# Optimization experiments

Measured on AMD Instinct MI355X. Metric: run time of the kernel, lower is better.

## Reference

```python
import jax, jax.numpy as jnp
import numpy as np

INPUT_DIM = 2048
NUM_EXPERTS = 64
TOP_K = 2


def setup_inputs() -> dict:
    key = jax.random.key(0)
    kx, kw = jax.random.split(key)
    x = jax.random.normal(kx, (4, 4096, INPUT_DIM), dtype=jnp.float32)
    # nn.Linear weight has shape [num_experts, input_dim]
    W = jax.random.normal(kw, (NUM_EXPERTS, INPUT_DIM), dtype=jnp.float32) * (INPUT_DIM ** -0.5)
    return {"x": x, "W": W}


def reference(x, W):
    # Flatten tokens: [N, D]
    x_flat = x.reshape(-1, INPUT_DIM)
    # Gate logits: [N, E]
    gate_logits = jnp.einsum("nd,ed->ne", x_flat, W)
    # Top-k (sorted descending, matching torch.topk)
    top_k_logits, top_k_indices = jax.lax.top_k(gate_logits, TOP_K)
    top_k_values = jax.nn.softmax(top_k_logits, axis=-1)
    return (top_k_indices, top_k_values)
```

## Files before the change

### kernel.cpp

```cpp
#include <hip/hip_runtime.h>
#include <hip/hip_bf16.h>
#include <math.h>

typedef float f4 __attribute__((ext_vector_type(4)));
typedef float f32x4 __attribute__((ext_vector_type(4)));
typedef short bf16x8 __attribute__((ext_vector_type(8)));
typedef unsigned int u32x4 __attribute__((ext_vector_type(4)));

#define D      2048
#define NE     64
#define TOKB   16
#define KSPLIT 8
#define KRNG   (D / KSPLIT)
#define KCH    32
#define NCH    (KRNG / KCH)
#define CSTR   68

__device__ __forceinline__ unsigned short bf16rne(float f) {
    unsigned int u = __builtin_bit_cast(unsigned int, f);
    u += 0x7fffu + ((u >> 16) & 1u);
    return (unsigned short)(u >> 16);
}
__device__ __forceinline__ float bf2f(unsigned short h) {
    unsigned int u = (unsigned int)h << 16;
    return __builtin_bit_cast(float, u);
}

__global__ __launch_bounds__(256)
void wprep(const float* __restrict__ W,
           unsigned short* __restrict__ Whp,
           unsigned short* __restrict__ Wlp)
{
    const int i  = blockIdx.x * 256 + threadIdx.x;
    const int j  = i & 7;
    const int l  = (i >> 3) & 63;
    const int et = (i >> 9) & 3;
    const int kc = i >> 11;
    const int e  = et * 16 + (l & 15);
    const int k  = kc * 32 + (l >> 4) * 8 + j;
    const float w = W[(size_t)e * D + k];
    const unsigned short h = bf16rne(w);
    Whp[i] = h;
    Wlp[i] = bf16rne(w - bf2f(h));
}

#define CVTPAIR(F0, F1, HOUT, LOUT) {                                        \
    __hip_bfloat162 hp_ = __float22bfloat162_rn(make_float2((F0), (F1)));    \
    unsigned hu_; __builtin_memcpy(&hu_, &hp_, 4);                           \
    const float h0_ = __builtin_bit_cast(float, hu_ << 16);                  \
    const float h1_ = __builtin_bit_cast(float, hu_ & 0xffff0000u);          \
    __hip_bfloat162 lp_ = __float22bfloat162_rn(                             \
        make_float2((F0) - h0_, (F1) - h1_));                                \
    unsigned lu_; __builtin_memcpy(&lu_, &lp_, 4);                           \
    HOUT = hu_;                                                              \
    LOUT = lu_;                                                              \
}

__global__ __launch_bounds__(512, 6)
void moe_fused(const float* __restrict__ x,
               const unsigned short* __restrict__ Whp,
               const unsigned short* __restrict__ Wlp,
               float* __restrict__ out, int ntok)
{
    __shared__ float cred[KSPLIT][TOKB * CSTR];

    const int t    = threadIdx.x;
    const int w    = t >> 6;
    const int l    = t & 63;
    const int tok0 = blockIdx.x * TOKB;

    const int ar  = l & 15;
    const int akb = (l >> 4) * 8;

    const float* xa = x + (size_t)(tok0 + ar) * D + w * KRNG + akb;
    const unsigned short* whp = Whp + (size_t)w * 16384 + l * 8;
    const unsigned short* wlp = Wlp + (size_t)w * 16384 + l * 8;

#define LOADX(ch, R0, R1) { \
    const float* p_ = xa + (ch) * KCH; \
    R0 = *(const f4*)(p_);     \
    R1 = *(const f4*)(p_ + 4); }

#define CHUNK(ch, R0, R1) { \
    bf16x8 bh[4], bl[4]; \
    _Pragma("unroll") \
    for (int et = 0; et < 4; ++et) { \
        const size_t o_ = (size_t)(4 * (ch) + et) * 512; \
        bh[et] = *(const bf16x8*)(whp + o_); \
        bl[et] = *(const bf16x8*)(wlp + o_); \
    } \
    unsigned hu0_, hu1_, hu2_, hu3_, lu0_, lu1_, lu2_, lu3_; \
    CVTPAIR(R0.x, R0.y, hu0_, lu0_); \
    CVTPAIR(R0.z, R0.w, hu1_, lu1_); \
    CVTPAIR(R1.x, R1.y, hu2_, lu2_); \
    CVTPAIR(R1.z, R1.w, hu3_, lu3_); \
    const u32x4 hv_ = {hu0_, hu1_, hu2_, hu3_}; \
    const u32x4 lv_ = {lu0_, lu1_, lu2_, lu3_}; \
    const bf16x8 ah = __builtin_bit_cast(bf16x8, hv_); \
    const bf16x8 al = __builtin_bit_cast(bf16x8, lv_); \
    if ((ch) + 2 < NCH) LOADX((ch) + 2, R0, R1); \
    _Pragma("unroll") \
    for (int et = 0; et < 4; ++et) { \
        acc[et] = __builtin_amdgcn_mfma_f32_16x16x32_bf16(ah, bh[et], acc[et], 0, 0, 0); \
        acc[et] = __builtin_amdgcn_mfma_f32_16x16x32_bf16(ah, bl[et], acc[et], 0, 0, 0); \
        acc[et] = __builtin_amdgcn_mfma_f32_16x16x32_bf16(al, bh[et], acc[et], 0, 0, 0); \
    } }

    const f32x4 zz = {0.f, 0.f, 0.f, 0.f};
    f32x4 acc[4] = {zz, zz, zz, zz};

    f4 xE0, xE1, xO0, xO1;

    LOADX(0, xE0, xE1);
    LOADX(1, xO0, xO1);

#pragma unroll
    for (int ch = 0; ch < NCH; ch += 2) {
        CHUNK(ch,     xE0, xE1);
        CHUNK(ch + 1, xO0, xO1);
    }

#undef LOADX
#undef CHUNK

#pragma unroll
    for (int et = 0; et < 4; ++et)
#pragma unroll
        for (int r = 0; r < 4; ++r) {
            const int tokl = (l >> 4) * 4 + r;
            cred[w][tokl * CSTR + et * 16 + (l & 15)] = acc[et][r];
        }
    __syncthreads();

    if (t < TOKB * 8) {
        const int tokl = t >> 3;
        const int eg   = t & 7;
        f4 s0 = {0.f,0.f,0.f,0.f}, s1 = {0.f,0.f,0.f,0.f};
#pragma unroll
        for (int ww = 0; ww < KSPLIT; ++ww) {
            const float* cw = &cred[ww][tokl * CSTR + eg * 8];
            s0 += *(const f4*)cw;
            s1 += *(const f4*)(cw + 4);
        }
        const float vv[8] = {s0.x, s0.y, s0.z, s0.w, s1.x, s1.y, s1.z, s1.w};
        float m1 = -INFINITY, m2 = -INFINITY;
        int i1 = 0, i2 = 0;
#pragma unroll
        for (int j = 0; j < 8; ++j) {
            const float v = vv[j];
            const int id = eg * 8 + j;
            if (v > m1)      { m2 = m1; i2 = i1; m1 = v; i1 = id; }
            else if (v > m2) { m2 = v;  i2 = id; }
        }
#pragma unroll
        for (int m = 1; m < 8; m <<= 1) {
            const float om1 = __shfl_xor(m1, m);
            const int   oi1 = __shfl_xor(i1, m);
            const float om2 = __shfl_xor(m2, m);
            const int   oi2 = __shfl_xor(i2, m);
            const bool b1 = (om1 > m1) || (om1 == m1 && oi1 < i1);
            const float c2v = b1 ? m1 : om1;  const int c2i = b1 ? i1 : oi1;
            const float c3v = b1 ? om2 : m2;  const int c3i = b1 ? oi2 : i2;
            if (b1) { m1 = om1; i1 = oi1; }
            const bool b2 = (c3v > c2v) || (c3v == c2v && c3i < c2i);
            m2 = b2 ? c3v : c2v;  i2 = b2 ? c3i : c2i;
        }
        if (eg == 0) {
            const int tok = tok0 + tokl;
            out[(size_t)tok * 2 + 0] = (float)i1;
            out[(size_t)tok * 2 + 1] = (float)i2;
            const float p1 = 1.0f / (1.0f + expf(m2 - m1));
            float* vals = out + (size_t)ntok * 2;
            vals[(size_t)tok * 2 + 0] = p1;
            vals[(size_t)tok * 2 + 1] = 1.0f - p1;
        }
    }
}

extern "C" void kernel_launch(void* const* d_in, const int* in_sizes, int n_in,
                              void* d_out, int out_size, void* d_ws, size_t ws_size,
                              hipStream_t stream)
{
    const float* x = (const float*)d_in[0];
    const float* W = (const float*)d_in[1];
    float* out = (float*)d_out;
    unsigned short* Whp = (unsigned short*)d_ws;
    unsigned short* Wlp = Whp + (size_t)NE * D;

    const int ntok = in_sizes[0] / D;
    wprep<<<(NE * D) / 256, 256, 0, stream>>>(W, Whp, Wlp);
    moe_fused<<<ntok / TOKB, 512, 0, stream>>>(x, Whp, Wlp, out, ntok);
}
```

Measured before the change: 46.24 us.

## Software-pipeline W and x loads with inline asm and explicit vmcnt waits

Replaces the compiler-scheduled loads in the main loop with inline-asm global_load_dwordx4 issues, double-buffering the weight fragments for the next chunk and keeping x loads two chunks ahead. Explicit s_waitcnt vmcnt(10) waits with sched barriers let the MFMAs of the current chunk overlap outstanding loads. The occupancy hint drops from 6 to 4 waves per SIMD to make room for the extra registers. Risks include wrong vmcnt accounting when the number of loads issued changes at the tail, and lower latency hiding from reduced occupancy.

```diff
diff --git a/kernel.cpp b/kernel.cpp
--- a/kernel.cpp
+++ b/kernel.cpp
@@ -56,7 +56,15 @@
     LOUT = lu_;                                                              \
 }
 
-__global__ __launch_bounds__(512, 6)
+#define GL16(dst, ptr) \
+    asm volatile("global_load_dwordx4 %0, %1, off" : "=v"(dst) : "v"(ptr) : "memory")
+
+#define WAIT10 { asm volatile("s_waitcnt vmcnt(10)" ::: "memory"); \
+                 __builtin_amdgcn_sched_barrier(0); }
+#define WAIT0  { asm volatile("s_waitcnt vmcnt(0)"  ::: "memory"); \
+                 __builtin_amdgcn_sched_barrier(0); }
+
+__global__ __launch_bounds__(512, 4)
 void moe_fused(const float* __restrict__ x,
                const unsigned short* __restrict__ Whp,
                const unsigned short* __restrict__ Wlp,
@@ -76,19 +84,28 @@
     const unsigned short* whp = Whp + (size_t)w * 16384 + l * 8;
     const unsigned short* wlp = Wlp + (size_t)w * 16384 + l * 8;
 
-#define LOADX(ch, R0, R1) { \
-    const float* p_ = xa + (ch) * KCH; \
-    R0 = *(const f4*)(p_);     \
-    R1 = *(const f4*)(p_ + 4); }
-
-#define CHUNK(ch, R0, R1) { \
-    bf16x8 bh[4], bl[4]; \
-    _Pragma("unroll") \
-    for (int et = 0; et < 4; ++et) { \
-        const size_t o_ = (size_t)(4 * (ch) + et) * 512; \
-        bh[et] = *(const bf16x8*)(whp + o_); \
-        bl[et] = *(const bf16x8*)(wlp + o_); \
-    } \
+    const f32x4 zz = {0.f, 0.f, 0.f, 0.f};
+    f32x4 acc[4] = {zz, zz, zz, zz};
+
+    bf16x8 bEh0, bEh1, bEh2, bEh3, bEl0, bEl1, bEl2, bEl3;
+    bf16x8 bOh0, bOh1, bOh2, bOh3, bOl0, bOl1, bOl2, bOl3;
+    f4 xE0, xE1, xO0, xO1;
+
+#define BISSUE(CH, S) { \
+    GL16(b##S##h0, whp + (size_t)(4*(CH)+0)*512); \
+    GL16(b##S##l0, wlp + (size_t)(4*(CH)+0)*512); \
+    GL16(b##S##h1, whp + (size_t)(4*(CH)+1)*512); \
+    GL16(b##S##l1, wlp + (size_t)(4*(CH)+1)*512); \
+    GL16(b##S##h2, whp + (size_t)(4*(CH)+2)*512); \
+    GL16(b##S##l2, wlp + (size_t)(4*(CH)+2)*512); \
+    GL16(b##S##h3, whp + (size_t)(4*(CH)+3)*512); \
+    GL16(b##S##l3, wlp + (size_t)(4*(CH)+3)*512); }
+
+#define XISSUE(CH, R0, R1) { \
+    GL16(R0, xa + (CH) * KCH);     \
+    GL16(R1, xa + (CH) * KCH + 4); }
+
+#define CVTA(R0, R1) \
     unsigned hu0_, hu1_, hu2_, hu3_, lu0_, lu1_, lu2_, lu3_; \
     CVTPAIR(R0.x, R0.y, hu0_, lu0_); \
     CVTPAIR(R0.z, R0.w, hu1_, lu1_); \
@@ -97,31 +114,60 @@
     const u32x4 hv_ = {hu0_, hu1_, hu2_, hu3_}; \
     const u32x4 lv_ = {lu0_, lu1_, lu2_, lu3_}; \
     const bf16x8 ah = __builtin_bit_cast(bf16x8, hv_); \
-    const bf16x8 al = __builtin_bit_cast(bf16x8, lv_); \
-    if ((ch) + 2 < NCH) LOADX((ch) + 2, R0, R1); \
-    _Pragma("unroll") \
-    for (int et = 0; et < 4; ++et) { \
-        acc[et] = __builtin_amdgcn_mfma_f32_16x16x32_bf16(ah, bh[et], acc[et], 0, 0, 0); \
-        acc[et] = __builtin_amdgcn_mfma_f32_16x16x32_bf16(ah, bl[et], acc[et], 0, 0, 0); \
-        acc[et] = __builtin_amdgcn_mfma_f32_16x16x32_bf16(al, bh[et], acc[et], 0, 0, 0); \
-    } }
-
-    const f32x4 zz = {0.f, 0.f, 0.f, 0.f};
-    f32x4 acc[4] = {zz, zz, zz, zz};
-
-    f4 xE0, xE1, xO0, xO1;
-
-    LOADX(0, xE0, xE1);
-    LOADX(1, xO0, xO1);
-
-#pragma unroll
-    for (int ch = 0; ch < NCH; ch += 2) {
-        CHUNK(ch,     xE0, xE1);
-        CHUNK(ch + 1, xO0, xO1);
-    }
-
-#undef LOADX
-#undef CHUNK
+    const bf16x8 al = __builtin_bit_cast(bf16x8, lv_);
+
+#define MFMAS(S) { \
+    acc[0] = __builtin_amdgcn_mfma_f32_16x16x32_bf16(ah, b##S##h0, acc[0], 0, 0, 0); \
+    acc[0] = __builtin_amdgcn_mfma_f32_16x16x32_bf16(ah, b##S##l0, acc[0], 0, 0, 0); \
+    acc[0] = __builtin_amdgcn_mfma_f32_16x16x32_bf16(al, b##S##h0, acc[0], 0, 0, 0); \
+    acc[1] = __builtin_amdgcn_mfma_f32_16x16x32_bf16(ah, b##S##h1, acc[1], 0, 0, 0); \
+    acc[1] = __builtin_amdgcn_mfma_f32_16x16x32_bf16(ah, b##S##l1, acc[1], 0, 0, 0); \
+    acc[1] = __builtin_amdgcn_mfma_f32_16x16x32_bf16(al, b##S##h1, acc[1], 0, 0, 0); \
+    acc[2] = __builtin_amdgcn_mfma_f32_16x16x32_bf16(ah, b##S##h2, acc[2], 0, 0, 0); \
+    acc[2] = __builtin_amdgcn_mfma_f32_16x16x32_bf16(ah, b##S##l2, acc[2], 0, 0, 0); \
+    acc[2] = __builtin_amdgcn_mfma_f32_16x16x32_bf16(al, b##S##h2, acc[2], 0, 0, 0); \
+    acc[3] = __builtin_amdgcn_mfma_f32_16x16x32_bf16(ah, b##S##h3, acc[3], 0, 0, 0); \
+    acc[3] = __builtin_amdgcn_mfma_f32_16x16x32_bf16(ah, b##S##l3, acc[3], 0, 0, 0); \
+    acc[3] = __builtin_amdgcn_mfma_f32_16x16x32_bf16(al, b##S##h3, acc[3], 0, 0, 0); }
+
+#define ITER_FULL(CH, S, OS, R0, R1) { \
+    BISSUE((CH) + 1, OS) \
+    WAIT10 \
+    CVTA(R0, R1) \
+    XISSUE((CH) + 2, R0, R1) \
+    MFMAS(S) }
+
+#define ITER_NOX(CH, S, OS, R0, R1) { \
+    BISSUE((CH) + 1, OS) \
+    WAIT10 \
+    CVTA(R0, R1) \
+    MFMAS(S) }
+
+#define ITER_LAST(CH, S, R0, R1) { \
+    WAIT0 \
+    CVTA(R0, R1) \
+    MFMAS(S) }
+
+    BISSUE(0, E)
+    XISSUE(0, xE0, xE1)
+    XISSUE(1, xO0, xO1)
+
+    ITER_FULL(0, E, O, xE0, xE1)
+    ITER_FULL(1, O, E, xO0, xO1)
+    ITER_FULL(2, E, O, xE0, xE1)
+    ITER_FULL(3, O, E, xO0, xO1)
+    ITER_FULL(4, E, O, xE0, xE1)
+    ITER_FULL(5, O, E, xO0, xO1)
+    ITER_NOX (6, E, O, xE0, xE1)
+    ITER_LAST(7, O, xO0, xO1)
+
+#undef BISSUE
+#undef XISSUE
+#undef CVTA
+#undef MFMAS
+#undef ITER_FULL
+#undef ITER_NOX
+#undef ITER_LAST
 
 #pragma unroll
     for (int et = 0; et < 4; ++et)
```

Result: no change. 45.52 us (-1.5%).

## Split gating GEMM into split-K kernel with LDS-shared weights plus top-2 pass

Applied to the files above, without the earlier changes.

The fused kernel is split into two kernels. The first is a split-K GEMM in which each 512-thread block covers 128 tokens (16 per wave) over one K slice. The block's W hi/lo slice is staged once in LDS with global_load_lds and shared by all eight waves, instead of every wave reading its own weights from global memory. Partial logits for each K slice go to a global workspace, and a second kernel sums the slices and performs top-2 plus softmax. This cuts redundant weight traffic per token, but adds a partial-sum round trip of 8x the logit size through global memory and one more kernel launch.

```diff
diff --git a/kernel.cpp b/kernel.cpp
--- a/kernel.cpp
+++ b/kernel.cpp
@@ -9,12 +9,16 @@
 
 #define D      2048
 #define NE     64
-#define TOKB   16
-#define KSPLIT 8
-#define KRNG   (D / KSPLIT)
+#define TPW    16
+#define NWAVE  8
+#define TOKB   (TPW * NWAVE)
+#define KS     8
+#define KRNG   (D / KS)
 #define KCH    32
 #define NCH    (KRNG / KCH)
-#define CSTR   68
+
+#define AS1C(p) ((const __attribute__((address_space(1))) void*)(p))
+#define AS3(p)  ((__attribute__((address_space(3))) void*)(p))
 
 __device__ __forceinline__ unsigned short bf16rne(float f) {
     unsigned int u = __builtin_bit_cast(unsigned int, f);
@@ -56,39 +60,51 @@
     LOUT = lu_;                                                              \
 }
 
-__global__ __launch_bounds__(512, 6)
-void moe_fused(const float* __restrict__ x,
-               const unsigned short* __restrict__ Whp,
-               const unsigned short* __restrict__ Wlp,
-               float* __restrict__ out, int ntok)
-{
-    __shared__ float cred[KSPLIT][TOKB * CSTR];
+__global__ __launch_bounds__(512, 4)
+void moe_gemm(const float* __restrict__ x,
+              const unsigned short* __restrict__ Whp,
+              const unsigned short* __restrict__ Wlp,
+              float* __restrict__ part, int ntok)
+{
+    __shared__ unsigned short Wlds[NCH][4][2][512];
 
     const int t    = threadIdx.x;
     const int w    = t >> 6;
     const int l    = t & 63;
-    const int tok0 = blockIdx.x * TOKB;
+    const int mbc  = ntok / TOKB;
+    const int mb   = blockIdx.x % mbc;
+    const int ks   = blockIdx.x / mbc;
+    const int tok0 = mb * TOKB;
 
     const int ar  = l & 15;
     const int akb = (l >> 4) * 8;
 
-    const float* xa = x + (size_t)(tok0 + ar) * D + w * KRNG + akb;
-    const unsigned short* whp = Whp + (size_t)w * 16384 + l * 8;
-    const unsigned short* wlp = Wlp + (size_t)w * 16384 + l * 8;
-
-#define LOADX(ch, R0, R1) { \
-    const float* p_ = xa + (ch) * KCH; \
-    R0 = *(const f4*)(p_);     \
-    R1 = *(const f4*)(p_ + 4); }
-
-#define CHUNK(ch, R0, R1) { \
-    bf16x8 bh[4], bl[4]; \
-    _Pragma("unroll") \
-    for (int et = 0; et < 4; ++et) { \
-        const size_t o_ = (size_t)(4 * (ch) + et) * 512; \
-        bh[et] = *(const bf16x8*)(whp + o_); \
-        bl[et] = *(const bf16x8*)(wlp + o_); \
-    } \
+    {
+        const size_t kcg = (size_t)(ks * NCH + w) * 4;
+#pragma unroll
+        for (int et = 0; et < 4; ++et) {
+            __builtin_amdgcn_global_load_lds(
+                AS1C(Whp + (kcg + et) * 512 + l * 8),
+                AS3(&Wlds[w][et][0][0]), 16, 0, 0);
+            __builtin_amdgcn_global_load_lds(
+                AS1C(Wlp + (kcg + et) * 512 + l * 8),
+                AS3(&Wlds[w][et][1][0]), 16, 0, 0);
+        }
+    }
+
+    const float* xa = x + (size_t)(tok0 + w * TPW + ar) * D + ks * KRNG + akb;
+
+    f4 xE0 = *(const f4*)(xa);
+    f4 xE1 = *(const f4*)(xa + 4);
+    f4 xO0 = *(const f4*)(xa + KCH);
+    f4 xO1 = *(const f4*)(xa + KCH + 4);
+
+    __syncthreads();
+
+    const f32x4 zz = {0.f, 0.f, 0.f, 0.f};
+    f32x4 acc[4] = {zz, zz, zz, zz};
+
+#define CVTA(R0, R1) \
     unsigned hu0_, hu1_, hu2_, hu3_, lu0_, lu1_, lu2_, lu3_; \
     CVTPAIR(R0.x, R0.y, hu0_, lu0_); \
     CVTPAIR(R0.z, R0.w, hu1_, lu1_); \
@@ -97,83 +113,86 @@
     const u32x4 hv_ = {hu0_, hu1_, hu2_, hu3_}; \
     const u32x4 lv_ = {lu0_, lu1_, lu2_, lu3_}; \
     const bf16x8 ah = __builtin_bit_cast(bf16x8, hv_); \
-    const bf16x8 al = __builtin_bit_cast(bf16x8, lv_); \
-    if ((ch) + 2 < NCH) LOADX((ch) + 2, R0, R1); \
+    const bf16x8 al = __builtin_bit_cast(bf16x8, lv_);
+
+#define CHUNK(CH, R0, R1, REFILL) { \
+    CVTA(R0, R1) \
+    if (REFILL) { R0 = *(const f4*)(xa + ((CH) + 2) * KCH); \
+                  R1 = *(const f4*)(xa + ((CH) + 2) * KCH + 4); } \
     _Pragma("unroll") \
     for (int et = 0; et < 4; ++et) { \
-        acc[et] = __builtin_amdgcn_mfma_f32_16x16x32_bf16(ah, bh[et], acc[et], 0, 0, 0); \
-        acc[et] = __builtin_amdgcn_mfma_f32_16x16x32_bf16(ah, bl[et], acc[et], 0, 0, 0); \
-        acc[et] = __builtin_amdgcn_mfma_f32_16x16x32_bf16(al, bh[et], acc[et], 0, 0, 0); \
+        const bf16x8 bh = *(const bf16x8*)&Wlds[CH][et][0][l * 8]; \
+        const bf16x8 bl = *(const bf16x8*)&Wlds[CH][et][1][l * 8]; \
+        acc[et] = __builtin_amdgcn_mfma_f32_16x16x32_bf16(ah, bh, acc[et], 0, 0, 0); \
+        acc[et] = __builtin_amdgcn_mfma_f32_16x16x32_bf16(ah, bl, acc[et], 0, 0, 0); \
+        acc[et] = __builtin_amdgcn_mfma_f32_16x16x32_bf16(al, bh, acc[et], 0, 0, 0); \
     } }
 
-    const f32x4 zz = {0.f, 0.f, 0.f, 0.f};
-    f32x4 acc[4] = {zz, zz, zz, zz};
-
-    f4 xE0, xE1, xO0, xO1;
-
-    LOADX(0, xE0, xE1);
-    LOADX(1, xO0, xO1);
-
-#pragma unroll
-    for (int ch = 0; ch < NCH; ch += 2) {
-        CHUNK(ch,     xE0, xE1);
-        CHUNK(ch + 1, xO0, xO1);
-    }
-
-#undef LOADX
+    CHUNK(0, xE0, xE1, 1)
+    CHUNK(1, xO0, xO1, 1)
+    CHUNK(2, xE0, xE1, 1)
+    CHUNK(3, xO0, xO1, 1)
+    CHUNK(4, xE0, xE1, 1)
+    CHUNK(5, xO0, xO1, 1)
+    CHUNK(6, xE0, xE1, 0)
+    CHUNK(7, xO0, xO1, 0)
+
+#undef CVTA
 #undef CHUNK
 
+    float* pp = part + ((size_t)ks * ntok + tok0 + w * TPW) * NE;
 #pragma unroll
     for (int et = 0; et < 4; ++et)
 #pragma unroll
-        for (int r = 0; r < 4; ++r) {
-            const int tokl = (l >> 4) * 4 + r;
-            cred[w][tokl * CSTR + et * 16 + (l & 15)] = acc[et][r];
-        }
-    __syncthreads();
-
-    if (t < TOKB * 8) {
-        const int tokl = t >> 3;
-        const int eg   = t & 7;
-        f4 s0 = {0.f,0.f,0.f,0.f}, s1 = {0.f,0.f,0.f,0.f};
-#pragma unroll
-        for (int ww = 0; ww < KSPLIT; ++ww) {
-            const float* cw = &cred[ww][tokl * CSTR + eg * 8];
-            s0 += *(const f4*)cw;
-            s1 += *(const f4*)(cw + 4);
-        }
-        const float vv[8] = {s0.x, s0.y, s0.z, s0.w, s1.x, s1.y, s1.z, s1.w};
-        float m1 = -INFINITY, m2 = -INFINITY;
-        int i1 = 0, i2 = 0;
-#pragma unroll
-        for (int j = 0; j < 8; ++j) {
-            const float v = vv[j];
-            const int id = eg * 8 + j;
-            if (v > m1)      { m2 = m1; i2 = i1; m1 = v; i1 = id; }
-            else if (v > m2) { m2 = v;  i2 = id; }
-        }
-#pragma unroll
-        for (int m = 1; m < 8; m <<= 1) {
-            const float om1 = __shfl_xor(m1, m);
-            const int   oi1 = __shfl_xor(i1, m);
-            const float om2 = __shfl_xor(m2, m);
-            const int   oi2 = __shfl_xor(i2, m);
-            const bool b1 = (om1 > m1) || (om1 == m1 && oi1 < i1);
-            const float c2v = b1 ? m1 : om1;  const int c2i = b1 ? i1 : oi1;
-            const float c3v = b1 ? om2 : m2;  const int c3i = b1 ? oi2 : i2;
-            if (b1) { m1 = om1; i1 = oi1; }
-            const bool b2 = (c3v > c2v) || (c3v == c2v && c3i < c2i);
-            m2 = b2 ? c3v : c2v;  i2 = b2 ? c3i : c2i;
-        }
-        if (eg == 0) {
-            const int tok = tok0 + tokl;
-            out[(size_t)tok * 2 + 0] = (float)i1;
-            out[(size_t)tok * 2 + 1] = (float)i2;
-            const float p1 = 1.0f / (1.0f + expf(m2 - m1));
-            float* vals = out + (size_t)ntok * 2;
-            vals[(size_t)tok * 2 + 0] = p1;
-            vals[(size_t)tok * 2 + 1] = 1.0f - p1;
-        }
+        for (int r = 0; r < 4; ++r)
+            pp[(size_t)((l >> 4) * 4 + r) * NE + et * 16 + (l & 15)] = acc[et][r];
+}
+
+__global__ __launch_bounds__(256)
+void moe_top2(const float* __restrict__ part,
+              float* __restrict__ out, int ntok)
+{
+    const int t   = threadIdx.x;
+    const int tok = blockIdx.x * 32 + (t >> 3);
+    const int eg  = t & 7;
+
+    f4 s0 = {0.f,0.f,0.f,0.f}, s1 = {0.f,0.f,0.f,0.f};
+#pragma unroll
+    for (int ks = 0; ks < KS; ++ks) {
+        const float* p = part + ((size_t)ks * ntok + tok) * NE + eg * 8;
+        s0 += *(const f4*)p;
+        s1 += *(const f4*)(p + 4);
+    }
+    const float vv[8] = {s0.x, s0.y, s0.z, s0.w, s1.x, s1.y, s1.z, s1.w};
+    float m1 = -INFINITY, m2 = -INFINITY;
+    int i1 = 0, i2 = 0;
+#pragma unroll
+    for (int j = 0; j < 8; ++j) {
+        const float v = vv[j];
+        const int id = eg * 8 + j;
+        if (v > m1)      { m2 = m1; i2 = i1; m1 = v; i1 = id; }
+        else if (v > m2) { m2 = v;  i2 = id; }
+    }
+#pragma unroll
+    for (int m = 1; m < 8; m <<= 1) {
+        const float om1 = __shfl_xor(m1, m);
+        const int   oi1 = __shfl_xor(i1, m);
+        const float om2 = __shfl_xor(m2, m);
+        const int   oi2 = __shfl_xor(i2, m);
+        const bool b1 = (om1 > m1) || (om1 == m1 && oi1 < i1);
+        const float c2v = b1 ? m1 : om1;  const int c2i = b1 ? i1 : oi1;
+        const float c3v = b1 ? om2 : m2;  const int c3i = b1 ? oi2 : i2;
+        if (b1) { m1 = om1; i1 = oi1; }
+        const bool b2 = (c3v > c2v) || (c3v == c2v && c3i < c2i);
+        m2 = b2 ? c3v : c2v;  i2 = b2 ? c3i : c2i;
+    }
+    if (eg == 0) {
+        out[(size_t)tok * 2 + 0] = (float)i1;
+        out[(size_t)tok * 2 + 1] = (float)i2;
+        const float p1 = 1.0f / (1.0f + expf(m2 - m1));
+        float* vals = out + (size_t)ntok * 2;
+        vals[(size_t)tok * 2 + 0] = p1;
+        vals[(size_t)tok * 2 + 1] = 1.0f - p1;
     }
 }
 
@@ -186,8 +205,10 @@
     float* out = (float*)d_out;
     unsigned short* Whp = (unsigned short*)d_ws;
     unsigned short* Wlp = Whp + (size_t)NE * D;
+    float* part = (float*)(Wlp + (size_t)NE * D);
 
     const int ntok = in_sizes[0] / D;
     wprep<<<(NE * D) / 256, 256, 0, stream>>>(W, Whp, Wlp);
-    moe_fused<<<ntok / TOKB, 512, 0, stream>>>(x, Whp, Wlp, out, ntok);
-}
+    moe_gemm<<<(ntok / TOKB) * KS, 512, 0, stream>>>(x, Whp, Wlp, part, ntok);
+    moe_top2<<<ntok / 32, 256, 0, stream>>>(part, out, ntok);
+}
```

Result: faster. 43.27 us (-6.4%).
